# Kernel tuning notes

Hardware: AMD Instinct MI355X
Metric: run time of the kernel (lower is better)

## Reference

```python
import jax, jax.numpy as jnp
import numpy as np

B, T, D = 8, 4096, 512
Q, K = 4, 1024
KERNEL, STRIDE = 5, 2
COMMIT = 0.25


def setup_inputs() -> dict:
    key = jax.random.key(0)
    k1, k2, k3 = jax.random.split(key, 3)
    x = jax.random.normal(k1, (B, T, D), dtype=jnp.float32)
    codebooks = jax.random.normal(k2, (Q, K, D), dtype=jnp.float32)
    # he_normal fan_in = KERNEL * D
    conv_w = jax.random.normal(k3, (KERNEL, D, D), dtype=jnp.float32) * np.sqrt(2.0 / (KERNEL * D))
    return {"x": x, "codebooks": codebooks, "conv_w": conv_w}


def _vq_nearest(residual, cb):
    # residual: [B,T,D], cb: [K,D] -> squared L2 distances [B,T,K]
    d = (jnp.sum(residual * residual, axis=-1, keepdims=True)
         - 2.0 * jnp.einsum('btd,kd->btk', residual, cb)
         + jnp.sum(cb * cb, axis=-1))
    idx = jnp.argmin(d, axis=-1)          # [B,T] int
    q = cb[idx]                            # [B,T,D] gather
    return q, idx


def residual_vq(x, codebooks):
    residual = x
    quantized_out = jnp.zeros_like(x)
    losses = []
    indices = []
    for qi in range(Q):  # small fixed number of quantizers
        q, idx = _vq_nearest(residual, codebooks[qi])
        # commitment loss (codebook frozen at inference / EMA-updated in training)
        losses.append(COMMIT * jnp.mean((jax.lax.stop_gradient(q) - residual) ** 2))
        # straight-through estimator
        q_st = residual + jax.lax.stop_gradient(q - residual)
        quantized_out = quantized_out + q_st
        residual = residual - jax.lax.stop_gradient(q)
        indices.append(idx)
    loss = jnp.sum(jnp.stack(losses))
    return quantized_out, jnp.stack(indices, axis=0), loss


def reference(x, codebooks, conv_w):
    quantized_out, indices, vq_loss = residual_vq(x, codebooks)
    # Conv1D, stride 2, 'same' padding, no bias: NWC x WIO -> NWC
    y = jax.lax.conv_general_dilated(
        quantized_out, conv_w,
        window_strides=(STRIDE,), padding='SAME',
        dimension_numbers=('NWC', 'WIO', 'NWC'))
    y = jax.nn.gelu(y, approximate=False)
    return y, quantized_out, indices, vq_loss
```

## Files before the change

### kernel.cpp

```cpp
#include <hip/hip_runtime.h>
#include <math.h>

#define Bq 8
#define Tq 4096
#define Dq 512
#define Qn 4
#define Kk 1024
#define OWn 2048
#define NROWS (Bq*Tq)

#define QO_OFF (Bq*OWn*Dq)
#define IDX_OFF (QO_OFF + Bq*Tq*Dq)
#define LOSS_OFF (IDX_OFF + Qn*NROWS)

typedef __bf16 bf16x8 __attribute__((ext_vector_type(8)));
typedef float f32x16 __attribute__((ext_vector_type(16)));
typedef float f32x4 __attribute__((ext_vector_type(4)));

__global__ __launch_bounds__(256) void prep_cb(const float* __restrict__ cb,
                                               float* __restrict__ cbnorm,
                                               __bf16* __restrict__ cbf,
                                               float* __restrict__ lacc) {
  int w = threadIdx.x >> 6, lane = threadIdx.x & 63;
  int row = blockIdx.x * 4 + w;
  int q = row >> 10, k = row & 1023;
  const f32x4* c4 = (const f32x4*)(cb + (size_t)row * Dq);
  f32x4 v0 = c4[lane * 2], v1 = c4[lane * 2 + 1];
  float s = v0.x*v0.x + v0.y*v0.y + v0.z*v0.z + v0.w*v0.w
          + v1.x*v1.x + v1.y*v1.y + v1.z*v1.z + v1.w*v1.w;
  bf16x8 bv;
  bv[0]=(__bf16)v0.x; bv[1]=(__bf16)v0.y; bv[2]=(__bf16)v0.z; bv[3]=(__bf16)v0.w;
  bv[4]=(__bf16)v1.x; bv[5]=(__bf16)v1.y; bv[6]=(__bf16)v1.z; bv[7]=(__bf16)v1.w;
  int ds = lane >> 1, hs = lane & 1;
  size_t off = ((size_t)((k >> 5) * 32 + ds) * 2 + hs) * 256 + (k & 31) * 8;
  *(bf16x8*)(cbf + (size_t)q * (Kk * Dq) + off) = bv;
#pragma unroll
  for (int off2 = 32; off2; off2 >>= 1) s += __shfl_down(s, off2);
  if (lane == 0) cbnorm[row] = s;
  if (blockIdx.x == 0 && threadIdx.x == 0) *lacc = 0.f;
}

__global__ __launch_bounds__(256) void prep_cmax(const float* __restrict__ cbnorm,
                                                 float* __restrict__ cmax) {
  int w = threadIdx.x >> 6, lane = threadIdx.x & 63;
  float m = 0.f;
#pragma unroll
  for (int j = 0; j < 16; ++j) m = fmaxf(m, cbnorm[w * Kk + lane * 16 + j]);
#pragma unroll
  for (int off = 32; off; off >>= 1) m = fmaxf(m, __shfl_down(m, off));
  if (lane == 0) cmax[w] = sqrtf(m);
}

__global__ __launch_bounds__(256) void prep_wb(const float* __restrict__ w,
                                               __bf16* __restrict__ wb) {
  int g = blockIdx.x * 256 + threadIdx.x;
  int l31 = g & 31, hs = (g >> 5) & 1, c32 = (g >> 6) & 15, s = g >> 10;
  int kw = s >> 5, ci16 = s & 31;
  int ci = ci16 * 16 + hs * 8;
  int co = c32 * 32 + l31;
  bf16x8 bv;
#pragma unroll
  for (int e = 0; e < 8; ++e)
    bv[e] = (__bf16)w[(size_t)(kw * Dq + ci + e) * Dq + co];
  *(bf16x8*)(wb + (size_t)g * 8) = bv;
}

__global__ __launch_bounds__(512, 2) void vq_all(
    const float* __restrict__ x, float* __restrict__ qo,
    const __bf16* __restrict__ cbf, const float* __restrict__ cb,
    const float* __restrict__ cbnorm, const float* __restrict__ cmax,
    float* __restrict__ idxo, float* __restrict__ lacc) {
  __shared__ __bf16 rh[32 * 512];
  __shared__ unsigned redB[32 * 8];
  __shared__ float rnorm_l[32];
  __shared__ float thrL[32];
  __shared__ int rowcount[32];
  __shared__ unsigned short rowlist[32 * 32];

  const int tid = threadIdx.x;
  const int w = tid >> 6, lane = tid & 63, l31 = lane & 31, hs = lane >> 5;
  const int row0g = blockIdx.x * 32;
  char* rhc = (char*)rh;

  f32x4 r0[4], r1[4];
#pragma unroll
  for (int rr = 0; rr < 4; ++rr) {
    size_t gb = (size_t)(row0g + w * 4 + rr) * Dq + lane * 8;
    r0[rr] = *(const f32x4*)(x + gb);
    r1[rr] = *(const f32x4*)(x + gb + 4);
  }
  float lsum = 0.f;

#pragma unroll 1
  for (int qi = 0; qi < Qn; ++qi) {
    const __bf16* cbf_q = cbf + (size_t)qi * (Kk * Dq);
    const float*  cb_q  = cb  + (size_t)qi * (Kk * Dq);
    const float*  cbn_q = cbnorm + qi * Kk;

#pragma unroll
    for (int rr = 0; rr < 4; ++rr) {
      int row = w * 4 + rr;
      bf16x8 bv;
      bv[0]=(__bf16)r0[rr].x; bv[1]=(__bf16)r0[rr].y;
      bv[2]=(__bf16)r0[rr].z; bv[3]=(__bf16)r0[rr].w;
      bv[4]=(__bf16)r1[rr].x; bv[5]=(__bf16)r1[rr].y;
      bv[6]=(__bf16)r1[rr].z; bv[7]=(__bf16)r1[rr].w;
      *(bf16x8*)(rhc + ((row * 1024 + lane * 16) ^ ((row & 7) << 4))) = bv;
      float rn = r0[rr].x*r0[rr].x + r0[rr].y*r0[rr].y + r0[rr].z*r0[rr].z + r0[rr].w*r0[rr].w
               + r1[rr].x*r1[rr].x + r1[rr].y*r1[rr].y + r1[rr].z*r1[rr].z + r1[rr].w*r1[rr].w;
#pragma unroll
      for (int off = 1; off < 64; off <<= 1) rn += __shfl_xor(rn, off);
      if (lane == 0) rnorm_l[row] = rn;
    }
    __syncthreads();

    unsigned ps[4][8];
    const int ab0 = l31 * 1024 + hs * 16;
    const int asw = (l31 & 7) << 4;
#pragma unroll
    for (int p = 0; p < 2; ++p) {
      const int ctA = 2 * p, ctB = 2 * p + 1;
      const __bf16* bpA = cbf_q + (size_t)(w * 4 + ctA) * 16384 + hs * 256 + l31 * 8;
      const __bf16* bpB = cbf_q + (size_t)(w * 4 + ctB) * 16384 + hs * 256 + l31 * 8;
      f32x16 accA, accB;
#pragma unroll
      for (int i = 0; i < 16; ++i) { accA[i] = 0.f; accB[i] = 0.f; }
#pragma unroll 8
      for (int ds = 0; ds < 32; ++ds) {
        bf16x8 a  = *(const bf16x8*)(rhc + ((ab0 + ds * 32) ^ asw));
        bf16x8 b0 = *(const bf16x8*)(bpA + ds * 512);
        bf16x8 b1 = *(const bf16x8*)(bpB + ds * 512);
        accA = __builtin_amdgcn_mfma_f32_32x32x16_bf16(a, b0, accA, 0, 0, 0);
        accB = __builtin_amdgcn_mfma_f32_32x32x16_bf16(a, b1, accB, 0, 0, 0);
      }
      const float cnA = cbn_q[w * 128 + ctA * 32 + l31];
      const float cnB = cbn_q[w * 128 + ctB * 32 + l31];
#pragma unroll
      for (int j = 0; j < 8; ++j) {
        __bf16 hA0 = (__bf16)(cnA - 2.f * accA[2 * j]);
        __bf16 hA1 = (__bf16)(cnA - 2.f * accA[2 * j + 1]);
        __bf16 hB0 = (__bf16)(cnB - 2.f * accB[2 * j]);
        __bf16 hB1 = (__bf16)(cnB - 2.f * accB[2 * j + 1]);
        ps[ctA][j] = (unsigned)__builtin_bit_cast(unsigned short, hA0)
                   | ((unsigned)__builtin_bit_cast(unsigned short, hA1) << 16);
        ps[ctB][j] = (unsigned)__builtin_bit_cast(unsigned short, hB0)
                   | ((unsigned)__builtin_bit_cast(unsigned short, hB1) << 16);
      }
    }

    unsigned pk[16];
#pragma unroll
    for (int i = 0; i < 16; ++i) {
      pk[i] = 0xFFFFFFFFu;
#pragma unroll
      for (int ct = 0; ct < 4; ++ct) {
        unsigned col = (unsigned)(w * 128 + ct * 32 + l31);
        unsigned u = (ps[ct][i >> 1] >> ((i & 1) * 16)) & 0xFFFFu;
        unsigned key = (u & 0x8000u) ? (u ^ 0xFFFFu) : (u | 0x8000u);
        unsigned pkc = (key << 10) | col;
        if (pkc < pk[i]) pk[i] = pkc;
      }
#pragma unroll
      for (int off = 1; off <= 16; off <<= 1) {
        unsigned t = __shfl_xor(pk[i], off);
        if (t < pk[i]) pk[i] = t;
      }
    }
    if (l31 == 0) {
#pragma unroll
      for (int i = 0; i < 16; ++i) {
        int rit = (i & 3) + 8 * (i >> 2) + 4 * hs;
        redB[rit * 8 + w] = pk[i];
      }
    }
    __syncthreads();

    if (tid < 32) {
      unsigned mb = redB[tid * 8];
#pragma unroll
      for (int j = 1; j < 8; ++j) {
        unsigned v = redB[tid * 8 + j];
        if (v < mb) mb = v;
      }
      unsigned key = (mb >> 10) & 0xFFFFu;
      unsigned ub = (key & 0x8000u) ? (key ^ 0x8000u) : (key ^ 0xFFFFu);
      float mstar = __uint_as_float(ub << 16);
      float rn = sqrtf(rnorm_l[tid]);
      float cm = cmax[qi];
      thrL[tid] = mstar + 0.025f * rn * cm + 0.0045f * cm * cm;
      rowcount[tid] = 0;
    }
    __syncthreads();

#pragma unroll
    for (int i = 0; i < 16; ++i) {
      int rit = (i & 3) + 8 * (i >> 2) + 4 * hs;
      float t = thrL[rit];
#pragma unroll
      for (int ct = 0; ct < 4; ++ct) {
        unsigned col = (unsigned)(w * 128 + ct * 32 + l31);
        unsigned u = (ps[ct][i >> 1] >> ((i & 1) * 16)) & 0xFFFFu;
        float s = __uint_as_float(u << 16);
        if (s <= t) {
          int p = atomicAdd(&rowcount[rit], 1);
          if (p < 32) rowlist[rit * 32 + p] = (unsigned short)col;
        }
      }
    }
    __syncthreads();

#pragma unroll
    for (int rr = 0; rr < 4; ++rr) {
      int row = w * 4 + rr;
      int cnt = rowcount[row];
      int total = (cnt > 32) ? Kk : cnt;
      float bs = 3.4028235e38f; int bk = 1 << 30;
      for (int ci2 = 0; ci2 < total; ++ci2) {
        int k = (cnt > 32) ? ci2 : (int)rowlist[row * 32 + ci2];
        const f32x4* crow = (const f32x4*)(cb_q + ((size_t)k << 9)) + lane * 2;
        f32x4 c0 = crow[0], c1 = crow[1];
        float dot = 0.f;
        dot = fmaf(r0[rr].x, c0.x, dot); dot = fmaf(r0[rr].y, c0.y, dot);
        dot = fmaf(r0[rr].z, c0.z, dot); dot = fmaf(r0[rr].w, c0.w, dot);
        dot = fmaf(r1[rr].x, c1.x, dot); dot = fmaf(r1[rr].y, c1.y, dot);
        dot = fmaf(r1[rr].z, c1.z, dot); dot = fmaf(r1[rr].w, c1.w, dot);
#pragma unroll
        for (int off = 1; off < 64; off <<= 1) dot += __shfl_xor(dot, off);
        float sc = cbn_q[k] - 2.f * dot;
        if (sc < bs || (sc == bs && k < bk)) { bs = sc; bk = k; }
      }
      if (lane == 0) idxo[(size_t)qi * NROWS + row0g + row] = (float)bk;
      const f32x4* crow = (const f32x4*)(cb_q + ((size_t)bk << 9)) + lane * 2;
      f32x4 c0 = crow[0], c1 = crow[1];
      r0[rr].x -= c0.x; r0[rr].y -= c0.y; r0[rr].z -= c0.z; r0[rr].w -= c0.w;
      r1[rr].x -= c1.x; r1[rr].y -= c1.y; r1[rr].z -= c1.z; r1[rr].w -= c1.w;
      lsum += r0[rr].x*r0[rr].x + r0[rr].y*r0[rr].y + r0[rr].z*r0[rr].z + r0[rr].w*r0[rr].w
            + r1[rr].x*r1[rr].x + r1[rr].y*r1[rr].y + r1[rr].z*r1[rr].z + r1[rr].w*r1[rr].w;
    }
    __syncthreads();
  }

#pragma unroll
  for (int rr = 0; rr < 4; ++rr) {
    size_t gb = (size_t)(row0g + w * 4 + rr) * Dq + lane * 8;
    f32x4 xv0 = *(const f32x4*)(x + gb), xv1 = *(const f32x4*)(x + gb + 4);
    f32x4 o0, o1;
    o0.x = xv0.x - r0[rr].x; o0.y = xv0.y - r0[rr].y;
    o0.z = xv0.z - r0[rr].z; o0.w = xv0.w - r0[rr].w;
    o1.x = xv1.x - r1[rr].x; o1.y = xv1.y - r1[rr].y;
    o1.z = xv1.z - r1[rr].z; o1.w = xv1.w - r1[rr].w;
    *(f32x4*)(qo + gb) = o0;
    *(f32x4*)(qo + gb + 4) = o1;
  }
#pragma unroll
  for (int off = 1; off < 64; off <<= 1) lsum += __shfl_xor(lsum, off);
  if (lane == 0) atomicAdd(lacc, lsum);
}

__global__ __launch_bounds__(512, 2) void conv_mfma(const float* __restrict__ qo,
                                                    const __bf16* __restrict__ wb,
                                                    float* __restrict__ y) {
  __shared__ char As[259 * 128];
  const int tid = threadIdx.x;
  const int w = tid >> 6, lane = tid & 63, l31 = lane & 31, hs = lane >> 5;
  const int rowblk = blockIdx.x, coblk = blockIdx.y;
  const int n = rowblk >> 4;
  const int o0 = (rowblk & 15) * 128;
  const int t0 = 2 * o0 - 1;
  const int c32g = coblk * 8 + w;

  f32x16 acc[4];
#pragma unroll
  for (int rt = 0; rt < 4; ++rt)
#pragma unroll
    for (int i = 0; i < 16; ++i) acc[rt][i] = 0.f;

  for (int ct8 = 0; ct8 < 8; ++ct8) {
    __syncthreads();
    for (int s = tid; s < 2072; s += 512) {
      int irow = s >> 3, cg = s & 7;
      int t = t0 + irow;
      bf16x8 bv;
      if (t >= 0 && t < Tq) {
        const float* src = qo + ((size_t)(n * Tq + t)) * Dq + ct8 * 64 + cg * 8;
        f32x4 v0 = *(const f32x4*)(src), v1 = *(const f32x4*)(src + 4);
        bv[0]=(__bf16)v0.x; bv[1]=(__bf16)v0.y; bv[2]=(__bf16)v0.z; bv[3]=(__bf16)v0.w;
        bv[4]=(__bf16)v1.x; bv[5]=(__bf16)v1.y; bv[6]=(__bf16)v1.z; bv[7]=(__bf16)v1.w;
      } else {
#pragma unroll
        for (int e = 0; e < 8; ++e) bv[e] = (__bf16)0.f;
      }
      *(bf16x8*)(As + ((irow * 128 + cg * 16) ^ (((irow >> 1) & 7) << 4))) = bv;
    }
    __syncthreads();
#pragma unroll
    for (int kw = 0; kw < 5; ++kw) {
#pragma unroll
      for (int ks = 0; ks < 4; ++ks) {
        int s16 = kw * 32 + ct8 * 4 + ks;
        bf16x8 b = *(const bf16x8*)(wb + ((size_t)(s16 * 16 + c32g) * 2 + hs) * 256 + l31 * 8);
#pragma unroll
        for (int rt = 0; rt < 4; ++rt) {
          int ir = 2 * (rt * 32 + l31) + kw;
          bf16x8 a = *(const bf16x8*)(As + ((ir * 128 + ks * 32 + hs * 16) ^ (((ir >> 1) & 7) << 4)));
          acc[rt] = __builtin_amdgcn_mfma_f32_32x32x16_bf16(a, b, acc[rt], 0, 0, 0);
        }
      }
    }
  }
  const int co = coblk * 256 + w * 32 + l31;
#pragma unroll
  for (int rt = 0; rt < 4; ++rt)
#pragma unroll
    for (int i = 0; i < 16; ++i) {
      int orow = rt * 32 + (i & 3) + 8 * (i >> 2) + 4 * hs;
      float v = acc[rt][i];
      float g = 0.5f * v * (1.f + erff(v * 0.70710678118654752f));
      y[((size_t)(n * OWn + o0 + orow)) * Dq + co] = g;
    }
}

__global__ void loss_final(const float* __restrict__ lacc, float* __restrict__ out) {
  out[0] = 0.25f * lacc[0] / 16777216.0f;
}

extern "C" void kernel_launch(void* const* d_in, const int* in_sizes, int n_in,
                              void* d_out, int out_size, void* d_ws, size_t ws_size,
                              hipStream_t stream) {
  const float* x  = (const float*)d_in[0];
  const float* cb = (const float*)d_in[1];
  const float* cw = (const float*)d_in[2];
  float* out = (float*)d_out;
  float* y    = out;
  float* qo   = out + QO_OFF;
  float* idxo = out + IDX_OFF;
  float* losso = out + LOSS_OFF;

  float* fws    = (float*)d_ws;
  float* lacc   = fws;
  float* cmax   = fws + 8;
  float* cbnorm = fws + 16;
  __bf16* cbf = (__bf16*)((char*)d_ws + (32 << 10));
  __bf16* wb  = (__bf16*)((char*)d_ws + (8 << 20));

  prep_cb<<<1024, 256, 0, stream>>>(cb, cbnorm, cbf, lacc);
  prep_cmax<<<1, 256, 0, stream>>>(cbnorm, cmax);
  prep_wb<<<640, 256, 0, stream>>>(cw, wb);

  vq_all<<<1024, 512, 0, stream>>>(x, qo, cbf, cb, cbnorm, cmax, idxo, lacc);

  conv_mfma<<<dim3(128, 2), 512, 0, stream>>>(qo, wb, y);
  loss_final<<<1, 1, 0, stream>>>(lacc, losso);
}
```

Measured before the change: 581.0 us.

## Use fp16 codebook MFMA with 64-row VQ tiles and tighter rescoring threshold

Switches the VQ distance GEMM from bf16 to fp16 operands. Each block now handles 64 rows instead of 32, so every codebook tile loaded from global memory feeds four MFMAs instead of two. The candidate threshold is recomputed around fp16 precision, which should shrink the number of codebook rows rescored exactly in fp32. The trade-offs are more registers (8 rows of residual per wave plus four accumulators), half as many blocks, and a risk that fp16 overflow or the fixed threshold constants miss the true argmin.

```diff
diff --git a/kernel.cpp b/kernel.cpp
--- a/kernel.cpp
+++ b/kernel.cpp
@@ -14,12 +14,18 @@
 #define LOSS_OFF (IDX_OFF + Qn*NROWS)
 
 typedef __bf16 bf16x8 __attribute__((ext_vector_type(8)));
+typedef _Float16 f16x8 __attribute__((ext_vector_type(8)));
 typedef float f32x16 __attribute__((ext_vector_type(16)));
 typedef float f32x4 __attribute__((ext_vector_type(4)));
 
+__device__ __forceinline__ unsigned pack2h(_Float16 a, _Float16 b) {
+  return (unsigned)__builtin_bit_cast(unsigned short, a)
+       | ((unsigned)__builtin_bit_cast(unsigned short, b) << 16);
+}
+
 __global__ __launch_bounds__(256) void prep_cb(const float* __restrict__ cb,
                                                float* __restrict__ cbnorm,
-                                               __bf16* __restrict__ cbf,
+                                               _Float16* __restrict__ cbf,
                                                float* __restrict__ lacc) {
   int w = threadIdx.x >> 6, lane = threadIdx.x & 63;
   int row = blockIdx.x * 4 + w;
@@ -28,12 +34,12 @@
   f32x4 v0 = c4[lane * 2], v1 = c4[lane * 2 + 1];
   float s = v0.x*v0.x + v0.y*v0.y + v0.z*v0.z + v0.w*v0.w
           + v1.x*v1.x + v1.y*v1.y + v1.z*v1.z + v1.w*v1.w;
-  bf16x8 bv;
-  bv[0]=(__bf16)v0.x; bv[1]=(__bf16)v0.y; bv[2]=(__bf16)v0.z; bv[3]=(__bf16)v0.w;
-  bv[4]=(__bf16)v1.x; bv[5]=(__bf16)v1.y; bv[6]=(__bf16)v1.z; bv[7]=(__bf16)v1.w;
+  f16x8 bv;
+  bv[0]=(_Float16)v0.x; bv[1]=(_Float16)v0.y; bv[2]=(_Float16)v0.z; bv[3]=(_Float16)v0.w;
+  bv[4]=(_Float16)v1.x; bv[5]=(_Float16)v1.y; bv[6]=(_Float16)v1.z; bv[7]=(_Float16)v1.w;
   int ds = lane >> 1, hs = lane & 1;
   size_t off = ((size_t)((k >> 5) * 32 + ds) * 2 + hs) * 256 + (k & 31) * 8;
-  *(bf16x8*)(cbf + (size_t)q * (Kk * Dq) + off) = bv;
+  *(f16x8*)(cbf + (size_t)q * (Kk * Dq) + off) = bv;
 #pragma unroll
   for (int off2 = 32; off2; off2 >>= 1) s += __shfl_down(s, off2);
   if (lane == 0) cbnorm[row] = s;
@@ -67,25 +73,25 @@
 
 __global__ __launch_bounds__(512, 2) void vq_all(
     const float* __restrict__ x, float* __restrict__ qo,
-    const __bf16* __restrict__ cbf, const float* __restrict__ cb,
+    const _Float16* __restrict__ cbf, const float* __restrict__ cb,
     const float* __restrict__ cbnorm, const float* __restrict__ cmax,
     float* __restrict__ idxo, float* __restrict__ lacc) {
-  __shared__ __bf16 rh[32 * 512];
-  __shared__ unsigned redB[32 * 8];
-  __shared__ float rnorm_l[32];
-  __shared__ float thrL[32];
-  __shared__ int rowcount[32];
-  __shared__ unsigned short rowlist[32 * 32];
+  __shared__ _Float16 rh[64 * 512];
+  __shared__ unsigned redB[64 * 8];
+  __shared__ float rnorm_l[64];
+  __shared__ float thrL[64];
+  __shared__ int rowcount[64];
+  __shared__ unsigned short rowlist[64 * 32];
 
   const int tid = threadIdx.x;
   const int w = tid >> 6, lane = tid & 63, l31 = lane & 31, hs = lane >> 5;
-  const int row0g = blockIdx.x * 32;
+  const int row0g = blockIdx.x * 64;
   char* rhc = (char*)rh;
 
-  f32x4 r0[4], r1[4];
-#pragma unroll
-  for (int rr = 0; rr < 4; ++rr) {
-    size_t gb = (size_t)(row0g + w * 4 + rr) * Dq + lane * 8;
+  f32x4 r0[8], r1[8];
+#pragma unroll
+  for (int rr = 0; rr < 8; ++rr) {
+    size_t gb = (size_t)(row0g + w * 8 + rr) * Dq + lane * 8;
     r0[rr] = *(const f32x4*)(x + gb);
     r1[rr] = *(const f32x4*)(x + gb + 4);
   }
@@ -93,19 +99,19 @@
 
 #pragma unroll 1
   for (int qi = 0; qi < Qn; ++qi) {
-    const __bf16* cbf_q = cbf + (size_t)qi * (Kk * Dq);
-    const float*  cb_q  = cb  + (size_t)qi * (Kk * Dq);
-    const float*  cbn_q = cbnorm + qi * Kk;
-
-#pragma unroll
-    for (int rr = 0; rr < 4; ++rr) {
-      int row = w * 4 + rr;
-      bf16x8 bv;
-      bv[0]=(__bf16)r0[rr].x; bv[1]=(__bf16)r0[rr].y;
-      bv[2]=(__bf16)r0[rr].z; bv[3]=(__bf16)r0[rr].w;
-      bv[4]=(__bf16)r1[rr].x; bv[5]=(__bf16)r1[rr].y;
-      bv[6]=(__bf16)r1[rr].z; bv[7]=(__bf16)r1[rr].w;
-      *(bf16x8*)(rhc + ((row * 1024 + lane * 16) ^ ((row & 7) << 4))) = bv;
+    const _Float16* cbf_q = cbf + (size_t)qi * (Kk * Dq);
+    const float*    cb_q  = cb  + (size_t)qi * (Kk * Dq);
+    const float*    cbn_q = cbnorm + qi * Kk;
+
+#pragma unroll
+    for (int rr = 0; rr < 8; ++rr) {
+      int row = w * 8 + rr;
+      f16x8 bv;
+      bv[0]=(_Float16)r0[rr].x; bv[1]=(_Float16)r0[rr].y;
+      bv[2]=(_Float16)r0[rr].z; bv[3]=(_Float16)r0[rr].w;
+      bv[4]=(_Float16)r1[rr].x; bv[5]=(_Float16)r1[rr].y;
+      bv[6]=(_Float16)r1[rr].z; bv[7]=(_Float16)r1[rr].w;
+      *(f16x8*)(rhc + ((row * 1024 + lane * 16) ^ ((row & 7) << 4))) = bv;
       float rn = r0[rr].x*r0[rr].x + r0[rr].y*r0[rr].y + r0[rr].z*r0[rr].z + r0[rr].w*r0[rr].w
                + r1[rr].x*r1[rr].x + r1[rr].y*r1[rr].y + r1[rr].z*r1[rr].z + r1[rr].w*r1[rr].w;
 #pragma unroll
@@ -114,68 +120,70 @@
     }
     __syncthreads();
 
-    unsigned ps[4][8];
+    unsigned psA[4][8], psB[4][8];
     const int ab0 = l31 * 1024 + hs * 16;
     const int asw = (l31 & 7) << 4;
 #pragma unroll
     for (int p = 0; p < 2; ++p) {
-      const int ctA = 2 * p, ctB = 2 * p + 1;
-      const __bf16* bpA = cbf_q + (size_t)(w * 4 + ctA) * 16384 + hs * 256 + l31 * 8;
-      const __bf16* bpB = cbf_q + (size_t)(w * 4 + ctB) * 16384 + hs * 256 + l31 * 8;
-      f32x16 accA, accB;
-#pragma unroll
-      for (int i = 0; i < 16; ++i) { accA[i] = 0.f; accB[i] = 0.f; }
+      const int ct0 = 2 * p, ct1 = 2 * p + 1;
+      const _Float16* bp0 = cbf_q + (size_t)(w * 4 + ct0) * 16384 + hs * 256 + l31 * 8;
+      const _Float16* bp1 = cbf_q + (size_t)(w * 4 + ct1) * 16384 + hs * 256 + l31 * 8;
+      f32x16 a00, a01, a10, a11;
+#pragma unroll
+      for (int i = 0; i < 16; ++i) { a00[i]=0.f; a01[i]=0.f; a10[i]=0.f; a11[i]=0.f; }
 #pragma unroll 8
       for (int ds = 0; ds < 32; ++ds) {
-        bf16x8 a  = *(const bf16x8*)(rhc + ((ab0 + ds * 32) ^ asw));
-        bf16x8 b0 = *(const bf16x8*)(bpA + ds * 512);
-        bf16x8 b1 = *(const bf16x8*)(bpB + ds * 512);
-        accA = __builtin_amdgcn_mfma_f32_32x32x16_bf16(a, b0, accA, 0, 0, 0);
-        accB = __builtin_amdgcn_mfma_f32_32x32x16_bf16(a, b1, accB, 0, 0, 0);
-      }
-      const float cnA = cbn_q[w * 128 + ctA * 32 + l31];
-      const float cnB = cbn_q[w * 128 + ctB * 32 + l31];
+        f16x8 a0 = *(const f16x8*)(rhc + ((ab0 + ds * 32) ^ asw));
+        f16x8 a1 = *(const f16x8*)(rhc + ((ab0 + 32 * 1024 + ds * 32) ^ asw));
+        f16x8 b0 = *(const f16x8*)(bp0 + ds * 512);
+        f16x8 b1 = *(const f16x8*)(bp1 + ds * 512);
+        a00 = __builtin_amdgcn_mfma_f32_32x32x16_f16(a0, b0, a00, 0, 0, 0);
+        a01 = __builtin_amdgcn_mfma_f32_32x32x16_f16(a0, b1, a01, 0, 0, 0);
+        a10 = __builtin_amdgcn_mfma_f32_32x32x16_f16(a1, b0, a10, 0, 0, 0);
+        a11 = __builtin_amdgcn_mfma_f32_32x32x16_f16(a1, b1, a11, 0, 0, 0);
+      }
+      const float cn0 = cbn_q[w * 128 + ct0 * 32 + l31];
+      const float cn1 = cbn_q[w * 128 + ct1 * 32 + l31];
 #pragma unroll
       for (int j = 0; j < 8; ++j) {
-        __bf16 hA0 = (__bf16)(cnA - 2.f * accA[2 * j]);
-        __bf16 hA1 = (__bf16)(cnA - 2.f * accA[2 * j + 1]);
-        __bf16 hB0 = (__bf16)(cnB - 2.f * accB[2 * j]);
-        __bf16 hB1 = (__bf16)(cnB - 2.f * accB[2 * j + 1]);
-        ps[ctA][j] = (unsigned)__builtin_bit_cast(unsigned short, hA0)
-                   | ((unsigned)__builtin_bit_cast(unsigned short, hA1) << 16);
-        ps[ctB][j] = (unsigned)__builtin_bit_cast(unsigned short, hB0)
-                   | ((unsigned)__builtin_bit_cast(unsigned short, hB1) << 16);
-      }
-    }
-
-    unsigned pk[16];
-#pragma unroll
-    for (int i = 0; i < 16; ++i) {
-      pk[i] = 0xFFFFFFFFu;
-#pragma unroll
-      for (int ct = 0; ct < 4; ++ct) {
-        unsigned col = (unsigned)(w * 128 + ct * 32 + l31);
-        unsigned u = (ps[ct][i >> 1] >> ((i & 1) * 16)) & 0xFFFFu;
-        unsigned key = (u & 0x8000u) ? (u ^ 0xFFFFu) : (u | 0x8000u);
-        unsigned pkc = (key << 10) | col;
-        if (pkc < pk[i]) pk[i] = pkc;
-      }
-#pragma unroll
-      for (int off = 1; off <= 16; off <<= 1) {
-        unsigned t = __shfl_xor(pk[i], off);
-        if (t < pk[i]) pk[i] = t;
-      }
-    }
-    if (l31 == 0) {
+        psA[ct0][j] = pack2h((_Float16)(cn0 - 2.f * a00[2*j]), (_Float16)(cn0 - 2.f * a00[2*j+1]));
+        psA[ct1][j] = pack2h((_Float16)(cn1 - 2.f * a01[2*j]), (_Float16)(cn1 - 2.f * a01[2*j+1]));
+        psB[ct0][j] = pack2h((_Float16)(cn0 - 2.f * a10[2*j]), (_Float16)(cn0 - 2.f * a10[2*j+1]));
+        psB[ct1][j] = pack2h((_Float16)(cn1 - 2.f * a11[2*j]), (_Float16)(cn1 - 2.f * a11[2*j+1]));
+      }
+    }
+
+#pragma unroll
+    for (int rt = 0; rt < 2; ++rt) {
+      unsigned pk[16];
 #pragma unroll
       for (int i = 0; i < 16; ++i) {
-        int rit = (i & 3) + 8 * (i >> 2) + 4 * hs;
-        redB[rit * 8 + w] = pk[i];
-      }
-    }
-    __syncthreads();
-
-    if (tid < 32) {
+        pk[i] = 0xFFFFFFFFu;
+#pragma unroll
+        for (int ct = 0; ct < 4; ++ct) {
+          unsigned col = (unsigned)(w * 128 + ct * 32 + l31);
+          unsigned u = ((rt == 0 ? psA[ct][i >> 1] : psB[ct][i >> 1]) >> ((i & 1) * 16)) & 0xFFFFu;
+          unsigned key = (u & 0x8000u) ? (u ^ 0xFFFFu) : (u | 0x8000u);
+          unsigned pkc = (key << 10) | col;
+          if (pkc < pk[i]) pk[i] = pkc;
+        }
+#pragma unroll
+        for (int off = 1; off <= 16; off <<= 1) {
+          unsigned t = __shfl_xor(pk[i], off);
+          if (t < pk[i]) pk[i] = t;
+        }
+      }
+      if (l31 == 0) {
+#pragma unroll
+        for (int i = 0; i < 16; ++i) {
+          int rit = rt * 32 + (i & 3) + 8 * (i >> 2) + 4 * hs;
+          redB[rit * 8 + w] = pk[i];
+        }
+      }
+    }
+    __syncthreads();
+
+    if (tid < 64) {
       unsigned mb = redB[tid * 8];
 #pragma unroll
       for (int j = 1; j < 8; ++j) {
@@ -184,34 +192,37 @@
       }
       unsigned key = (mb >> 10) & 0xFFFFu;
       unsigned ub = (key & 0x8000u) ? (key ^ 0x8000u) : (key ^ 0xFFFFu);
-      float mstar = __uint_as_float(ub << 16);
+      float mstar = (float)__builtin_bit_cast(_Float16, (unsigned short)ub);
       float rn = sqrtf(rnorm_l[tid]);
       float cm = cmax[qi];
-      thrL[tid] = mstar + 0.025f * rn * cm + 0.0045f * cm * cm;
+      thrL[tid] = mstar + 0.005f * rn * cm + 0.001f * fabsf(mstar) + 0.3f;
       rowcount[tid] = 0;
     }
     __syncthreads();
 
 #pragma unroll
-    for (int i = 0; i < 16; ++i) {
-      int rit = (i & 3) + 8 * (i >> 2) + 4 * hs;
-      float t = thrL[rit];
-#pragma unroll
-      for (int ct = 0; ct < 4; ++ct) {
-        unsigned col = (unsigned)(w * 128 + ct * 32 + l31);
-        unsigned u = (ps[ct][i >> 1] >> ((i & 1) * 16)) & 0xFFFFu;
-        float s = __uint_as_float(u << 16);
-        if (s <= t) {
-          int p = atomicAdd(&rowcount[rit], 1);
-          if (p < 32) rowlist[rit * 32 + p] = (unsigned short)col;
-        }
-      }
-    }
-    __syncthreads();
-
-#pragma unroll
-    for (int rr = 0; rr < 4; ++rr) {
-      int row = w * 4 + rr;
+    for (int rt = 0; rt < 2; ++rt) {
+#pragma unroll
+      for (int i = 0; i < 16; ++i) {
+        int rit = rt * 32 + (i & 3) + 8 * (i >> 2) + 4 * hs;
+        float t = thrL[rit];
+#pragma unroll
+        for (int ct = 0; ct < 4; ++ct) {
+          unsigned col = (unsigned)(w * 128 + ct * 32 + l31);
+          unsigned u = ((rt == 0 ? psA[ct][i >> 1] : psB[ct][i >> 1]) >> ((i & 1) * 16)) & 0xFFFFu;
+          float s = (float)__builtin_bit_cast(_Float16, (unsigned short)u);
+          if (s <= t) {
+            int p = atomicAdd(&rowcount[rit], 1);
+            if (p < 32) rowlist[rit * 32 + p] = (unsigned short)col;
+          }
+        }
+      }
+    }
+    __syncthreads();
+
+#pragma unroll
+    for (int rr = 0; rr < 8; ++rr) {
+      int row = w * 8 + rr;
       int cnt = rowcount[row];
       int total = (cnt > 32) ? Kk : cnt;
       float bs = 3.4028235e38f; int bk = 1 << 30;
@@ -241,8 +252,8 @@
   }
 
 #pragma unroll
-  for (int rr = 0; rr < 4; ++rr) {
-    size_t gb = (size_t)(row0g + w * 4 + rr) * Dq + lane * 8;
+  for (int rr = 0; rr < 8; ++rr) {
+    size_t gb = (size_t)(row0g + w * 8 + rr) * Dq + lane * 8;
     f32x4 xv0 = *(const f32x4*)(x + gb), xv1 = *(const f32x4*)(x + gb + 4);
     f32x4 o0, o1;
     o0.x = xv0.x - r0[rr].x; o0.y = xv0.y - r0[rr].y;
@@ -340,14 +351,14 @@
   float* lacc   = fws;
   float* cmax   = fws + 8;
   float* cbnorm = fws + 16;
-  __bf16* cbf = (__bf16*)((char*)d_ws + (32 << 10));
+  _Float16* cbf = (_Float16*)((char*)d_ws + (32 << 10));
   __bf16* wb  = (__bf16*)((char*)d_ws + (8 << 20));
 
   prep_cb<<<1024, 256, 0, stream>>>(cb, cbnorm, cbf, lacc);
   prep_cmax<<<1, 256, 0, stream>>>(cbnorm, cmax);
   prep_wb<<<640, 256, 0, stream>>>(cw, wb);
 
-  vq_all<<<1024, 512, 0, stream>>>(x, qo, cbf, cb, cbnorm, cmax, idxo, lacc);
+  vq_all<<<512, 512, 0, stream>>>(x, qo, cbf, cb, cbnorm, cmax, idxo, lacc);
 
   conv_mfma<<<dim3(128, 2), 512, 0, stream>>>(qo, wb, y);
   loss_final<<<1, 1, 0, stream>>>(lacc, losso);
```

Measured after the change: 502.3 us. 1.16x faster.
